# Kernel tuning notes

Hardware: AMD Instinct MI355X
Metric: run time of the kernel (lower is better)

Reference implementation:

```python
import jax, jax.numpy as jnp
import numpy as np

AXIS = 4  # axis_neuron


def silu(x):
    return x * jax.nn.sigmoid(x)


def setup_inputs() -> dict:
    key = jax.random.key(0)
    ks = jax.random.split(key, 20)
    nf, nloc, nall, nnei, a_sel = 1, 1024, 1024, 64, 20
    n_dim, e_dim, a_dim = 128, 64, 64
    f32 = jnp.float32

    def W(k, i, o):
        return jax.random.normal(k, (i, o), f32) / np.float32(np.sqrt(i))

    angle_in = a_dim + n_dim + 2 * e_dim  # angle_dim with a_compress_rate=0, a_mess_has_n=True
    return {
        "node_ebd_ext": jax.random.normal(ks[0], (nf, nall, n_dim), f32),
        "edge_ebd": jax.random.normal(ks[1], (nf, nloc, nnei, e_dim), f32),
        "h2": jax.random.normal(ks[2], (nf, nloc, nnei, 3), f32),
        "angle_ebd": jax.random.normal(ks[3], (nf, nloc, a_sel, a_sel, a_dim), f32),
        "sw": jax.random.uniform(ks[4], (nf, nloc, nnei), f32),
        "a_sw": jax.random.uniform(ks[5], (nf, nloc, a_sel), f32),
        "W_self": W(ks[6], n_dim, n_dim), "b_self": jnp.zeros((n_dim,), f32),
        "W_sym": W(ks[7], (e_dim + n_dim) * AXIS, n_dim), "b_sym": jnp.zeros((n_dim,), f32),
        "W_ne": W(ks[8], 2 * n_dim + e_dim, n_dim), "b_ne": jnp.zeros((n_dim,), f32),
        "W_es": W(ks[9], 2 * n_dim + e_dim, e_dim), "b_es": jnp.zeros((e_dim,), f32),
        "W_ea1": W(ks[10], angle_in, e_dim), "b_ea1": jnp.zeros((e_dim,), f32),
        "W_ea2": W(ks[11], e_dim, e_dim), "b_ea2": jnp.zeros((e_dim,), f32),
        "W_as": W(ks[12], angle_in, a_dim), "b_as": jnp.zeros((a_dim,), f32),
        "res_n": jnp.full((3, n_dim), 0.1, f32),
        "res_e": jnp.full((2, e_dim), 0.1, f32),
        "res_a": jnp.full((1, a_dim), 0.1, f32),
        "nlist": jax.random.randint(ks[13], (nf, nloc, nnei), 0, nall),
        "nlist_mask": jnp.ones((nf, nloc, nnei), bool),
        "a_nlist_mask": jnp.ones((nf, nloc, a_sel), bool),
    }


def _forward(node_ebd_ext, edge_ebd, h2, angle_ebd, sw, a_sw,
             W_self, b_self, W_sym, b_sym, W_ne, b_ne, W_es, b_es,
             W_ea1, b_ea1, W_ea2, b_ea2, W_as, b_as, res_n, res_e, res_a,
             nlist, nlist_mask, a_nlist_mask):
    nf, nloc, nnei, e_dim = edge_ebd.shape
    a_sel = angle_ebd.shape[2]
    a_dim = angle_ebd.shape[-1]
    n_dim = node_ebd_ext.shape[-1]
    node_ebd = node_ebd_ext[:, :nloc]  # nf x nloc x n_dim

    sw = jnp.where(nlist_mask, sw, 0.0)          # masked switch
    a_sw = jnp.where(a_nlist_mask, a_sw, 0.0)

    # gather neighbor node embeddings: nf x nloc x nnei x n_dim
    idx = jnp.where(nlist_mask, nlist, 0)
    nei_node = jnp.take_along_axis(
        node_ebd_ext, idx.reshape(nf, nloc * nnei)[..., None], axis=1
    ).reshape(nf, nloc, nnei, n_dim)

    # node self mlp
    n_self = silu(node_ebd @ W_self + b_self)

    # symmetrization op: hg = h^T g / nnei; grrg = hg[:axis]^T hg / 3
    def grrg(g):
        gw = g * sw[..., None]
        hg = jnp.einsum('flnt,flnd->fltd', h2, gw) / nnei       # f l 3 d
        out = jnp.einsum('flta,fltd->flad', hg[..., :AXIS], hg) / 3.0
        return out.reshape(nf, nloc, -1)                        # f l (axis*d)

    node_sym = silu(jnp.concatenate([grrg(edge_ebd), grrg(nei_node)], axis=-1) @ W_sym + b_sym)

    # node-edge message: linear over concat([node_i, node_j, edge]) = sum of blocks
    W0, W1, W2 = W_ne[:n_dim], W_ne[n_dim:2 * n_dim], W_ne[2 * n_dim:]
    pre_ne = (node_ebd @ W0)[:, :, None, :] + nei_node @ W1 + edge_ebd @ W2 + b_ne
    n_edge = jnp.sum(silu(pre_ne) * sw[..., None], axis=-2) / nnei

    node_new = node_ebd + res_n[0] * n_self + res_n[1] * node_sym + res_n[2] * n_edge

    # edge self message (same edge_info)
    V0, V1, V2 = W_es[:n_dim], W_es[n_dim:2 * n_dim], W_es[2 * n_dim:]
    edge_self = silu((node_ebd @ V0)[:, :, None, :] + nei_node @ V1 + edge_ebd @ V2 + b_es)

    # ---- angle path ----
    e_ang = jnp.where(a_nlist_mask[..., None], edge_ebd[:, :, :a_sel], 0.0)  # f l a e
    s0, s1, s2 = a_dim, a_dim + n_dim, a_dim + n_dim + e_dim
    A0, A1, A2, A3 = W_ea1[:s0], W_ea1[s0:s1], W_ea1[s1:s2], W_ea1[s2:]
    # angle_info @ W_ea1 without materializing the concat (blocks broadcast)
    pre_ang = (angle_ebd @ A0
               + (node_ebd @ A1)[:, :, None, None, :]
               + (e_ang @ A2)[:, :, None, :, :]   # edge_for_angle_i varies along axis 3
               + (e_ang @ A3)[:, :, :, None, :]   # edge_for_angle_j varies along axis 2
               + b_ea1)
    e_ang_upd = silu(pre_ang)                                     # f l a a e
    weighted = a_sw[:, :, :, None, None] * a_sw[:, :, None, :, None] * e_ang_upd
    reduced = jnp.sum(weighted, axis=-2) / np.float32(np.sqrt(a_sel))  # f l a e
    padded = jnp.pad(reduced, ((0, 0), (0, 0), (0, nnei - a_sel), (0, 0)))
    e_angle_msg = silu(padded @ W_ea2 + b_ea2)
    edge_new = edge_ebd + res_e[0] * edge_self + res_e[1] * e_angle_msg

    # angle self update (same angle_info)
    B0, B1, B2, B3 = W_as[:s0], W_as[s0:s1], W_as[s1:s2], W_as[s2:]
    angle_self = silu(angle_ebd @ B0
                      + (node_ebd @ B1)[:, :, None, None, :]
                      + (e_ang @ B2)[:, :, None, :, :]
                      + (e_ang @ B3)[:, :, :, None, :]
                      + b_as)
    angle_new = angle_ebd + res_a[0] * angle_self
    return node_new, edge_new, angle_new


def reference(node_ebd_ext, edge_ebd, h2, angle_ebd, sw, a_sw,
              W_self, b_self, W_sym, b_sym, W_ne, b_ne, W_es, b_es,
              W_ea1, b_ea1, W_ea2, b_ea2, W_as, b_as, res_n, res_e, res_a,
              nlist, nlist_mask, a_nlist_mask):
    return _forward(node_ebd_ext, edge_ebd, h2, angle_ebd, sw, a_sw,
                    W_self, b_self, W_sym, b_sym, W_ne, b_ne, W_es, b_es,
                    W_ea1, b_ea1, W_ea2, b_ea2, W_as, b_as, res_n, res_e, res_a,
                    nlist, nlist_mask, a_nlist_mask)
```

## Files before the change

### kernel.cpp

```cpp
#include <hip/hip_runtime.h>

#define DEVINL __device__ __forceinline__

#define NLOC 1024
#define NNEI 64
#define NDIM 128
#define EDIM 64
#define ADIM 64
#define ASEL 20

enum : size_t {
  WS_NSELF = 0,
  WS_NW0   = WS_NSELF + 1024*128,
  WS_NV0   = WS_NW0   + 1024*128,
  WS_NA1   = WS_NV0   + 1024*64,
  WS_NB1   = WS_NA1   + 1024*64,
  WS_PA2   = WS_NB1   + 1024*64,
  WS_PA3   = WS_PA2   + 1024*ASEL*64,
  WS_PB2   = WS_PA3   + 1024*ASEL*64,
  WS_PB3   = WS_PB2   + 1024*ASEL*64,
  WS_F32_END = WS_PB3 + 1024*ASEL*64
};
__device__ float g_ws[WS_F32_END];
__device__ float g_red[1024*ASEL*64];

DEVINL float siluf(float x) {
  return x * __builtin_amdgcn_rcpf(1.0f + __expf(-x));
}

__global__ __launch_bounds__(128) void k0_node_pre(
    const float* __restrict__ node,
    const float* __restrict__ W_self, const float* __restrict__ b_self,
    const float* __restrict__ W_ne,   const float* __restrict__ b_ne,
    const float* __restrict__ W_es,   const float* __restrict__ b_es,
    const float* __restrict__ W_ea1,  const float* __restrict__ b_ea1,
    const float* __restrict__ W_as,   const float* __restrict__ b_as)
{
  const int l = blockIdx.x, t = threadIdx.x;
  __shared__ float nl[128];
  nl[t] = node[l*128 + t];
  __syncthreads();
  float aS = b_self[t];
  float aW = b_ne[t];
  #pragma unroll 8
  for (int k = 0; k < 128; ++k) {
    float nv = nl[k];
    aS = fmaf(nv, W_self[k*128 + t], aS);
    aW = fmaf(nv, W_ne[k*128 + t], aW);
  }
  g_ws[WS_NSELF + l*128 + t] = siluf(aS);
  g_ws[WS_NW0   + l*128 + t] = aW;
  if (t < 64) {
    float aV = b_es[t], aA = b_ea1[t], aB = b_as[t];
    #pragma unroll 8
    for (int k = 0; k < 128; ++k) {
      float nv = nl[k];
      aV = fmaf(nv, W_es[k*64 + t], aV);
      aA = fmaf(nv, W_ea1[(64 + k)*64 + t], aA);
      aB = fmaf(nv, W_as[(64 + k)*64 + t], aB);
    }
    g_ws[WS_NV0 + l*64 + t] = aV;
    g_ws[WS_NA1 + l*64 + t] = aA;
    g_ws[WS_NB1 + l*64 + t] = aB;
  }
}

__global__ __launch_bounds__(256) void kp_proj(
    const float* __restrict__ edge,
    const float* __restrict__ W_ea1, const float* __restrict__ W_as)
{
  const int l = blockIdx.x, t = threadIdx.x;
  __shared__ float eang[ASEL*65];
  for (int e = t; e < ASEL*64; e += 256)
    eang[(e >> 6)*65 + (e & 63)] = edge[(size_t)l*4096 + e];
  __syncthreads();
  const int o = t & 63, wv = t >> 6;
  #pragma unroll 1
  for (int m = 0; m < 4; ++m) {
    const float* __restrict__ Wp =
          (m == 0) ? (W_ea1 + 192*64)
        : (m == 1) ? (W_ea1 + 256*64)
        : (m == 2) ? (W_as  + 192*64)
        :            (W_as  + 256*64);
    float* __restrict__ outp = g_ws +
          ((m == 0) ? WS_PA2 : (m == 1) ? WS_PA3 : (m == 2) ? WS_PB2 : WS_PB3)
        + (size_t)l*ASEL*64;
    float a0 = 0.f, a1 = 0.f, a2 = 0.f, a3 = 0.f, a4 = 0.f;
    #pragma unroll 4
    for (int k = 0; k < 64; ++k) {
      float w = Wp[k*64 + o];
      a0 = fmaf(eang[(wv     )*65 + k], w, a0);
      a1 = fmaf(eang[(wv +  4)*65 + k], w, a1);
      a2 = fmaf(eang[(wv +  8)*65 + k], w, a2);
      a3 = fmaf(eang[(wv + 12)*65 + k], w, a3);
      a4 = fmaf(eang[(wv + 16)*65 + k], w, a4);
    }
    outp[(wv     )*64 + o] = a0;
    outp[(wv +  4)*64 + o] = a1;
    outp[(wv +  8)*64 + o] = a2;
    outp[(wv + 12)*64 + o] = a3;
    outp[(wv + 16)*64 + o] = a4;
  }
}

__global__ __launch_bounds__(256, 4) void k2_angle(
    const float* __restrict__ ang,
    const float* __restrict__ a_sw,
    const float* __restrict__ res_a,
    const float* __restrict__ W_ea1, const float* __restrict__ W_as,
    float* __restrict__ angle_out)
{
  const int bid = blockIdx.x;
  const int l = bid / 5, b = bid % 5;
  const int t = threadIdx.x;

  __shared__ __align__(16) float angl[80*68];
  __shared__ __align__(16) float eA2l[ASEL*68], eB2l[ASEL*68];
  __shared__ float aswl[ASEL];

  const float* __restrict__ angbase = ang + ((size_t)l*400 + b*80)*64;
  #pragma unroll
  for (int q = 0; q < 5; ++q) {
    int g = t + q*256;
    int lr = g >> 4, c4 = g & 15;
    float4 v = reinterpret_cast<const float4*>(angbase)[g];
    *reinterpret_cast<float4*>(&angl[lr*68 + c4*4]) = v;
  }
  {
    const float* __restrict__ pa2 = g_ws + WS_PA2 + (size_t)l*ASEL*64;
    const float* __restrict__ pb2 = g_ws + WS_PB2 + (size_t)l*ASEL*64;
    for (int g = t; g < ASEL*16; g += 256) {
      int j = g >> 4, c4 = g & 15;
      *reinterpret_cast<float4*>(&eA2l[j*68 + c4*4]) =
          reinterpret_cast<const float4*>(pa2)[g];
      *reinterpret_cast<float4*>(&eB2l[j*68 + c4*4]) =
          reinterpret_cast<const float4*>(pb2)[g];
    }
  }
  if (t < ASEL) aswl[t] = a_sw[l*ASEL + t];

  const int cg = t & 15, rg = t >> 4;
  const int c0 = cg*4;
  const int i_loc = rg >> 2;
  const int i = b*4 + i_loc;
  const int lr0 = rg*5;

  float4 nA1v = *reinterpret_cast<const float4*>(g_ws + WS_NA1 + l*64 + c0);
  float4 nB1v = *reinterpret_cast<const float4*>(g_ws + WS_NB1 + l*64 + c0);
  float4 eA3v = *reinterpret_cast<const float4*>(g_ws + WS_PA3 + ((size_t)l*ASEL + i)*64 + c0);
  float4 eB3v = *reinterpret_cast<const float4*>(g_ws + WS_PB3 + ((size_t)l*ASEL + i)*64 + c0);
  float4 resav = *reinterpret_cast<const float4*>(res_a + c0);

  __syncthreads();

  const float* __restrict__ A0g = W_ea1;
  const float* __restrict__ B0g = W_as;

  float accA[20], accB[20];
  #pragma unroll
  for (int q = 0; q < 20; ++q) { accA[q] = 0.f; accB[q] = 0.f; }

  #pragma unroll 2
  for (int k = 0; k < 64; k += 4) {
    float vr[5][4];
    #pragma unroll
    for (int q = 0; q < 5; ++q)
      *reinterpret_cast<float4*>(vr[q]) =
          *reinterpret_cast<const float4*>(&angl[(lr0 + q)*68 + k]);
    #pragma unroll
    for (int kk = 0; kk < 4; ++kk) {
      float4 wA = *reinterpret_cast<const float4*>(A0g + (size_t)(k + kk)*64 + c0);
      float4 wB = *reinterpret_cast<const float4*>(B0g + (size_t)(k + kk)*64 + c0);
      #pragma unroll
      for (int q = 0; q < 5; ++q) {
        float av = vr[q][kk];
        accA[q*4+0] = fmaf(av, wA.x, accA[q*4+0]);
        accA[q*4+1] = fmaf(av, wA.y, accA[q*4+1]);
        accA[q*4+2] = fmaf(av, wA.z, accA[q*4+2]);
        accA[q*4+3] = fmaf(av, wA.w, accA[q*4+3]);
        accB[q*4+0] = fmaf(av, wB.x, accB[q*4+0]);
        accB[q*4+1] = fmaf(av, wB.y, accB[q*4+1]);
        accB[q*4+2] = fmaf(av, wB.z, accB[q*4+2]);
        accB[q*4+3] = fmaf(av, wB.w, accB[q*4+3]);
      }
    }
  }

  float red0 = 0.f, red1 = 0.f, red2 = 0.f, red3 = 0.f;
  #pragma unroll
  for (int q = 0; q < 5; ++q) {
    int lr = lr0 + q;
    int j = lr - i_loc*20;
    float aswj = aswl[j];
    float4 e2A = *reinterpret_cast<const float4*>(&eA2l[j*68 + c0]);
    float4 e2B = *reinterpret_cast<const float4*>(&eB2l[j*68 + c0]);
    float4 orig = *reinterpret_cast<const float4*>(&angl[lr*68 + c0]);

    float pA0 = accA[q*4+0] + nA1v.x + e2A.x + eA3v.x;
    float pA1 = accA[q*4+1] + nA1v.y + e2A.y + eA3v.y;
    float pA2 = accA[q*4+2] + nA1v.z + e2A.z + eA3v.z;
    float pA3 = accA[q*4+3] + nA1v.w + e2A.w + eA3v.w;
    red0 = fmaf(aswj, siluf(pA0), red0);
    red1 = fmaf(aswj, siluf(pA1), red1);
    red2 = fmaf(aswj, siluf(pA2), red2);
    red3 = fmaf(aswj, siluf(pA3), red3);

    float pB0 = accB[q*4+0] + nB1v.x + e2B.x + eB3v.x;
    float pB1 = accB[q*4+1] + nB1v.y + e2B.y + eB3v.y;
    float pB2 = accB[q*4+2] + nB1v.z + e2B.z + eB3v.z;
    float pB3 = accB[q*4+3] + nB1v.w + e2B.w + eB3v.w;
    float4 outv;
    outv.x = orig.x + resav.x * siluf(pB0);
    outv.y = orig.y + resav.y * siluf(pB1);
    outv.z = orig.z + resav.z * siluf(pB2);
    outv.w = orig.w + resav.w * siluf(pB3);
    *reinterpret_cast<float4*>(angle_out + ((size_t)l*400 + b*80 + lr)*64 + c0) = outv;
  }

  red0 += __shfl_xor(red0, 16); red0 += __shfl_xor(red0, 32);
  red1 += __shfl_xor(red1, 16); red1 += __shfl_xor(red1, 32);
  red2 += __shfl_xor(red2, 16); red2 += __shfl_xor(red2, 32);
  red3 += __shfl_xor(red3, 16); red3 += __shfl_xor(red3, 32);
  if ((t & 0x30) == 0) {
    float sc = aswl[i] * 0.22360679775f;
    float4 o4 = make_float4(red0*sc, red1*sc, red2*sc, red3*sc);
    *reinterpret_cast<float4*>(g_red + ((size_t)l*ASEL + i)*64 + c0) = o4;
  }
}

__global__ __launch_bounds__(256, 2) void k3_node_edge(
    const float* __restrict__ node_ext,
    const float* __restrict__ edge,
    const float* __restrict__ h2,
    const float* __restrict__ sw,
    const int* __restrict__ nlist,
    const float* __restrict__ W_sym, const float* __restrict__ b_sym,
    const float* __restrict__ W_ne,  const float* __restrict__ W_es,
    const float* __restrict__ W_ea2, const float* __restrict__ b_ea2,
    const float* __restrict__ res_n, const float* __restrict__ res_e,
    float* __restrict__ node_out,
    float* __restrict__ edge_out)
{
  const int l = blockIdx.x, t = threadIdx.x;
  __shared__ __align__(16) float AL[64*196];
  __shared__ __align__(16) float WL[16*192];
  __shared__ float hwv[64*4];
  __shared__ float swl[64];
  __shared__ float hgE[3*64], hgN[3*128];
  __shared__ float cat[768];
  __shared__ float nsym[128];
  __shared__ float msgl[ASEL*64];
  __shared__ float msgc[64];
  __shared__ float redn[128];
  __shared__ int   idxl[64];

  if (t < 64) idxl[t] = nlist[l*64 + t];
  if (t >= 64 && t < 192) redn[t - 64] = 0.f;
  if (t < 64) {
    float s = sw[l*64 + t];
    swl[t] = s;
    hwv[t*4+0] = h2[(l*64 + t)*3 + 0] * s;
    hwv[t*4+1] = h2[(l*64 + t)*3 + 1] * s;
    hwv[t*4+2] = h2[(l*64 + t)*3 + 2] * s;
  }
  __syncthreads();

  for (int g = t; g < 2048; g += 256) {
    int n = g >> 5, q = g & 31;
    float4 v = *reinterpret_cast<const float4*>(node_ext + (size_t)idxl[n]*128 + q*4);
    *reinterpret_cast<float4*>(&AL[n*196 + q*4]) = v;
  }
  for (int g = t; g < 1024; g += 256) {
    int n = g >> 4, q = g & 15;
    float4 v = *reinterpret_cast<const float4*>(edge + (size_t)l*4096 + n*64 + q*4);
    *reinterpret_cast<float4*>(&AL[n*196 + 128 + q*4]) = v;
  }
  __syncthreads();

  for (int e = t; e < 192; e += 256) {
    int tt = e >> 6, d = e & 63;
    float acc = 0.f;
    #pragma unroll 4
    for (int n = 0; n < 64; ++n) acc = fmaf(hwv[n*4 + tt], AL[n*196 + 128 + d], acc);
    hgE[tt*64 + d] = acc * (1.f/64.f);
  }
  for (int e = t; e < 384; e += 256) {
    int tt = e >> 7, k = e & 127;
    float acc = 0.f;
    #pragma unroll 4
    for (int n = 0; n < 64; ++n) acc = fmaf(hwv[n*4 + tt], AL[n*196 + k], acc);
    hgN[tt*128 + k] = acc * (1.f/64.f);
  }
  __syncthreads();

  for (int e = t; e < 256; e += 256) {
    int a = e >> 6, d = e & 63;
    cat[e] = (hgE[a]*hgE[d] + hgE[64 + a]*hgE[64 + d] + hgE[128 + a]*hgE[128 + d]) * (1.f/3.f);
  }
  for (int e = t; e < 512; e += 256) {
    int a = e >> 7, k = e & 127;
    cat[256 + e] = (hgN[a]*hgN[k] + hgN[128 + a]*hgN[128 + k] + hgN[256 + a]*hgN[256 + k]) * (1.f/3.f);
  }
  __syncthreads();

  if (t < 128) {
    float acc = b_sym[t];
    #pragma unroll 4
    for (int c = 0; c < 768; ++c)
      acc = fmaf(cat[c], W_sym[c*128 + t], acc);
    nsym[t] = siluf(acc);
  } else {
    int idx = t - 128;
    if (idx < 64) msgc[idx] = siluf(b_ea2[idx]);
    for (int q = 0; q < 10; ++q) {
      int e = q*128 + idx;
      int n = e >> 6, oo = e & 63;
      float acc = b_ea2[oo];
      #pragma unroll 4
      for (int k = 0; k < 64; ++k)
        acc = fmaf(g_red[((size_t)l*ASEL + n)*64 + k], W_ea2[k*64 + oo], acc);
      msgl[e] = siluf(acc);
    }
  }

  const int tx = t & 15, ty = t >> 4;
  const int n0 = ty*4, c0 = tx*12;

  float acc[4][12];
  #pragma unroll
  for (int r = 0; r < 4; ++r)
    #pragma unroll
    for (int cc = 0; cc < 12; ++cc) acc[r][cc] = 0.f;

  float4 wreg[3];
  #pragma unroll
  for (int q = 0; q < 3; ++q) {
    int g = q*256 + t;
    int kk = g / 48, c4 = g % 48;
    int c = c4*4, krow = 128 + kk;
    wreg[q] = (c < 128)
        ? *reinterpret_cast<const float4*>(W_ne + (size_t)krow*128 + c)
        : *reinterpret_cast<const float4*>(W_es + (size_t)krow*64 + (c - 128));
  }

  #pragma unroll 1
  for (int kb = 0; kb < 12; ++kb) {
    __syncthreads();
    #pragma unroll
    for (int q = 0; q < 3; ++q) {
      int g = q*256 + t;
      int kk = g / 48, c4 = g % 48;
      *reinterpret_cast<float4*>(&WL[kk*192 + c4*4]) = wreg[q];
    }
    if (kb < 11) {
      #pragma unroll
      for (int q = 0; q < 3; ++q) {
        int g = q*256 + t;
        int kk = g / 48, c4 = g % 48;
        int c = c4*4, krow = 128 + (kb + 1)*16 + kk;
        wreg[q] = (c < 128)
            ? *reinterpret_cast<const float4*>(W_ne + (size_t)krow*128 + c)
            : *reinterpret_cast<const float4*>(W_es + (size_t)krow*64 + (c - 128));
      }
    }
    __syncthreads();

    const int kbase = kb*16;
    #pragma unroll
    for (int kk = 0; kk < 16; kk += 4) {
      float ar[4][4];
      #pragma unroll
      for (int r = 0; r < 4; ++r)
        *reinterpret_cast<float4*>(ar[r]) =
            *reinterpret_cast<const float4*>(&AL[(n0 + r)*196 + kbase + kk]);
      #pragma unroll
      for (int j = 0; j < 4; ++j) {
        float4 w0 = *reinterpret_cast<const float4*>(&WL[(kk + j)*192 + c0]);
        float4 w1 = *reinterpret_cast<const float4*>(&WL[(kk + j)*192 + c0 + 4]);
        float4 w2 = *reinterpret_cast<const float4*>(&WL[(kk + j)*192 + c0 + 8]);
        #pragma unroll
        for (int r = 0; r < 4; ++r) {
          float av = ar[r][j];
          acc[r][0]  = fmaf(av, w0.x, acc[r][0]);
          acc[r][1]  = fmaf(av, w0.y, acc[r][1]);
          acc[r][2]  = fmaf(av, w0.z, acc[r][2]);
          acc[r][3]  = fmaf(av, w0.w, acc[r][3]);
          acc[r][4]  = fmaf(av, w1.x, acc[r][4]);
          acc[r][5]  = fmaf(av, w1.y, acc[r][5]);
          acc[r][6]  = fmaf(av, w1.z, acc[r][6]);
          acc[r][7]  = fmaf(av, w1.w, acc[r][7]);
          acc[r][8]  = fmaf(av, w2.x, acc[r][8]);
          acc[r][9]  = fmaf(av, w2.y, acc[r][9]);
          acc[r][10] = fmaf(av, w2.z, acc[r][10]);
          acc[r][11] = fmaf(av, w2.w, acc[r][11]);
        }
      }
    }
  }

  float colb[12];
  #pragma unroll
  for (int cc = 0; cc < 12; ++cc) {
    int c = c0 + cc;
    colb[cc] = (c < 128) ? g_ws[WS_NW0 + l*128 + c]
                         : g_ws[WS_NV0 + l*64 + (c - 128)];
  }
  float np[12];
  #pragma unroll
  for (int cc = 0; cc < 12; ++cc) np[cc] = 0.f;

  #pragma unroll
  for (int r = 0; r < 4; ++r) {
    int n = n0 + r;
    float sn = swl[n];
    #pragma unroll
    for (int cc = 0; cc < 12; ++cc) {
      int c = c0 + cc;
      float s = siluf(acc[r][cc] + colb[cc]);
      if (c < 128) {
        np[cc] = fmaf(s, sn, np[cc]);
      } else {
        int o = c - 128;
        float msgv = (n < ASEL) ? msgl[n*64 + o] : msgc[o];
        float ef = AL[n*196 + 128 + o];
        edge_out[(size_t)l*4096 + n*64 + o] =
            ef + res_e[o]*s + res_e[64 + o]*msgv;
      }
    }
  }

  #pragma unroll
  for (int cc = 0; cc < 12; ++cc) {
    np[cc] += __shfl_xor(np[cc], 16);
    np[cc] += __shfl_xor(np[cc], 32);
  }
  if ((ty & 3) == 0) {
    #pragma unroll
    for (int cc = 0; cc < 12; ++cc) {
      int c = c0 + cc;
      if (c < 128) atomicAdd(&redn[c], np[cc]);
    }
  }
  __syncthreads();

  if (t < 128) {
    const int c = t;
    float nedge = redn[c] * (1.f/64.f);
    float nodev = node_ext[l*128 + c];
    node_out[l*128 + c] = nodev + res_n[c]*g_ws[WS_NSELF + l*128 + c]
                        + res_n[128 + c]*nsym[c] + res_n[256 + c]*nedge;
  }
}

extern "C" void kernel_launch(void* const* d_in, const int* in_sizes, int n_in,
                              void* d_out, int out_size, void* d_ws, size_t ws_size,
                              hipStream_t stream) {
  const float* node_ext = (const float*)d_in[0];
  const float* edge_ebd = (const float*)d_in[1];
  const float* h2       = (const float*)d_in[2];
  const float* angle    = (const float*)d_in[3];
  const float* sw       = (const float*)d_in[4];
  const float* a_sw     = (const float*)d_in[5];
  const float* W_self   = (const float*)d_in[6];
  const float* b_self   = (const float*)d_in[7];
  const float* W_sym    = (const float*)d_in[8];
  const float* b_sym    = (const float*)d_in[9];
  const float* W_ne     = (const float*)d_in[10];
  const float* b_ne     = (const float*)d_in[11];
  const float* W_es     = (const float*)d_in[12];
  const float* b_es     = (const float*)d_in[13];
  const float* W_ea1    = (const float*)d_in[14];
  const float* b_ea1    = (const float*)d_in[15];
  const float* W_ea2    = (const float*)d_in[16];
  const float* b_ea2    = (const float*)d_in[17];
  const float* W_as     = (const float*)d_in[18];
  const float* b_as     = (const float*)d_in[19];
  const float* res_n    = (const float*)d_in[20];
  const float* res_e    = (const float*)d_in[21];
  const float* res_a    = (const float*)d_in[22];
  const int*   nlist    = (const int*)d_in[23];

  float* out = (float*)d_out;
  float* node_out  = out;
  float* edge_out  = out + 1024*128;
  float* angle_out = out + 1024*128 + (size_t)1024*64*64;

  k0_node_pre<<<1024, 128, 0, stream>>>(node_ext, W_self, b_self, W_ne, b_ne,
                                        W_es, b_es, W_ea1, b_ea1, W_as, b_as);
  kp_proj<<<1024, 256, 0, stream>>>(edge_ebd, W_ea1, W_as);
  k2_angle<<<1024*5, 256, 0, stream>>>(angle, a_sw, res_a,
                                       W_ea1, W_as, angle_out);
  k3_node_edge<<<1024, 256, 0, stream>>>(node_ext, edge_ebd, h2, sw, nlist,
                                         W_sym, b_sym, W_ne, W_es, W_ea2, b_ea2,
                                         res_n, res_e, node_out, edge_out);
}
```

Before: 653.0 us.

## Merge node-pre and edge projection kernels; split symmetry/message work out of node-edge kernel

```diff
diff --git a/kernel.cpp b/kernel.cpp
--- a/kernel.cpp
+++ b/kernel.cpp
@@ -19,7 +19,9 @@
   WS_PA3   = WS_PA2   + 1024*ASEL*64,
   WS_PB2   = WS_PA3   + 1024*ASEL*64,
   WS_PB3   = WS_PB2   + 1024*ASEL*64,
-  WS_F32_END = WS_PB3 + 1024*ASEL*64
+  WS_NSYM  = WS_PB3   + 1024*ASEL*64,
+  WS_MSG   = WS_NSYM  + 1024*128,
+  WS_F32_END = WS_MSG + 1024*21*64
 };
 __device__ float g_ws[WS_F32_END];
 __device__ float g_red[1024*ASEL*64];
@@ -28,8 +30,9 @@
   return x * __builtin_amdgcn_rcpf(1.0f + __expf(-x));
 }
 
-__global__ __launch_bounds__(128) void k0_node_pre(
+__global__ __launch_bounds__(256) void k01_pre(
     const float* __restrict__ node,
+    const float* __restrict__ edge,
     const float* __restrict__ W_self, const float* __restrict__ b_self,
     const float* __restrict__ W_ne,   const float* __restrict__ b_ne,
     const float* __restrict__ W_es,   const float* __restrict__ b_es,
@@ -38,42 +41,38 @@
 {
   const int l = blockIdx.x, t = threadIdx.x;
   __shared__ float nl[128];
-  nl[t] = node[l*128 + t];
-  __syncthreads();
-  float aS = b_self[t];
-  float aW = b_ne[t];
-  #pragma unroll 8
-  for (int k = 0; k < 128; ++k) {
-    float nv = nl[k];
-    aS = fmaf(nv, W_self[k*128 + t], aS);
-    aW = fmaf(nv, W_ne[k*128 + t], aW);
-  }
-  g_ws[WS_NSELF + l*128 + t] = siluf(aS);
-  g_ws[WS_NW0   + l*128 + t] = aW;
-  if (t < 64) {
-    float aV = b_es[t], aA = b_ea1[t], aB = b_as[t];
+  __shared__ float eang[ASEL*65];
+  if (t < 128) nl[t] = node[l*128 + t];
+  for (int e = t; e < ASEL*64; e += 256)
+    eang[(e >> 6)*65 + (e & 63)] = edge[(size_t)l*4096 + e];
+  __syncthreads();
+
+  if (t < 128) {
+    float aS = b_self[t];
+    float aW = b_ne[t];
     #pragma unroll 8
     for (int k = 0; k < 128; ++k) {
       float nv = nl[k];
-      aV = fmaf(nv, W_es[k*64 + t], aV);
-      aA = fmaf(nv, W_ea1[(64 + k)*64 + t], aA);
-      aB = fmaf(nv, W_as[(64 + k)*64 + t], aB);
-    }
-    g_ws[WS_NV0 + l*64 + t] = aV;
-    g_ws[WS_NA1 + l*64 + t] = aA;
-    g_ws[WS_NB1 + l*64 + t] = aB;
-  }
-}
-
-__global__ __launch_bounds__(256) void kp_proj(
-    const float* __restrict__ edge,
-    const float* __restrict__ W_ea1, const float* __restrict__ W_as)
-{
-  const int l = blockIdx.x, t = threadIdx.x;
-  __shared__ float eang[ASEL*65];
-  for (int e = t; e < ASEL*64; e += 256)
-    eang[(e >> 6)*65 + (e & 63)] = edge[(size_t)l*4096 + e];
-  __syncthreads();
+      aS = fmaf(nv, W_self[k*128 + t], aS);
+      aW = fmaf(nv, W_ne[k*128 + t], aW);
+    }
+    g_ws[WS_NSELF + l*128 + t] = siluf(aS);
+    g_ws[WS_NW0   + l*128 + t] = aW;
+    if (t < 64) {
+      float aV = b_es[t], aA = b_ea1[t], aB = b_as[t];
+      #pragma unroll 8
+      for (int k = 0; k < 128; ++k) {
+        float nv = nl[k];
+        aV = fmaf(nv, W_es[k*64 + t], aV);
+        aA = fmaf(nv, W_ea1[(64 + k)*64 + t], aA);
+        aB = fmaf(nv, W_as[(64 + k)*64 + t], aB);
+      }
+      g_ws[WS_NV0 + l*64 + t] = aV;
+      g_ws[WS_NA1 + l*64 + t] = aA;
+      g_ws[WS_NB1 + l*64 + t] = aB;
+    }
+  }
+
   const int o = t & 63, wv = t >> 6;
   #pragma unroll 1
   for (int m = 0; m < 4; ++m) {
@@ -228,15 +227,96 @@
   }
 }
 
-__global__ __launch_bounds__(256, 2) void k3_node_edge(
+__global__ __launch_bounds__(256) void kn_sym(
     const float* __restrict__ node_ext,
     const float* __restrict__ edge,
     const float* __restrict__ h2,
     const float* __restrict__ sw,
     const int* __restrict__ nlist,
     const float* __restrict__ W_sym, const float* __restrict__ b_sym,
+    const float* __restrict__ W_ea2, const float* __restrict__ b_ea2)
+{
+  const int l = blockIdx.x, t = threadIdx.x;
+  __shared__ float hwv[64*4];
+  __shared__ int   idxl[64];
+  __shared__ float gredl[ASEL*64];
+  __shared__ float hgE[3*64], hgN[3*128];
+  __shared__ float cat[768];
+  __shared__ float nsymp[2][128];
+
+  if (t < 64) {
+    idxl[t] = nlist[l*64 + t];
+    float s = sw[l*64 + t];
+    hwv[t*4+0] = h2[(l*64 + t)*3 + 0] * s;
+    hwv[t*4+1] = h2[(l*64 + t)*3 + 1] * s;
+    hwv[t*4+2] = h2[(l*64 + t)*3 + 2] * s;
+  }
+  for (int e = t; e < ASEL*64; e += 256)
+    gredl[e] = g_red[(size_t)l*ASEL*64 + e];
+  __syncthreads();
+
+  for (int e = t; e < 576; e += 256) {
+    if (e < 192) {
+      int tt = e >> 6, d = e & 63;
+      float acc = 0.f;
+      #pragma unroll 4
+      for (int n = 0; n < 64; ++n)
+        acc = fmaf(hwv[n*4 + tt], edge[(size_t)l*4096 + n*64 + d], acc);
+      hgE[tt*64 + d] = acc * (1.f/64.f);
+    } else {
+      int e2 = e - 192;
+      int tt = e2 >> 7, k = e2 & 127;
+      float acc = 0.f;
+      #pragma unroll 4
+      for (int n = 0; n < 64; ++n)
+        acc = fmaf(hwv[n*4 + tt], node_ext[(size_t)idxl[n]*128 + k], acc);
+      hgN[tt*128 + k] = acc * (1.f/64.f);
+    }
+  }
+  __syncthreads();
+
+  {
+    int e = t;
+    int a = e >> 6, d = e & 63;
+    cat[e] = (hgE[a]*hgE[d] + hgE[64 + a]*hgE[64 + d] + hgE[128 + a]*hgE[128 + d]) * (1.f/3.f);
+  }
+  for (int e = t; e < 512; e += 256) {
+    int a = e >> 7, k = e & 127;
+    cat[256 + e] = (hgN[a]*hgN[k] + hgN[128 + a]*hgN[128 + k] + hgN[256 + a]*hgN[256 + k]) * (1.f/3.f);
+  }
+  __syncthreads();
+
+  {
+    const int c = t & 127, half = t >> 7;
+    const int k0 = half*384;
+    float acc = half ? 0.f : b_sym[c];
+    #pragma unroll 8
+    for (int k = 0; k < 384; ++k)
+      acc = fmaf(cat[k0 + k], W_sym[(size_t)(k0 + k)*128 + c], acc);
+    nsymp[half][c] = acc;
+  }
+  __syncthreads();
+  if (t < 128)
+    g_ws[WS_NSYM + l*128 + t] = siluf(nsymp[0][t] + nsymp[1][t]);
+
+  for (int e = t; e < 21*64; e += 256) {
+    int n = e >> 6, o = e & 63;
+    float acc = b_ea2[o];
+    if (n < ASEL) {
+      #pragma unroll 4
+      for (int k = 0; k < 64; ++k)
+        acc = fmaf(gredl[n*64 + k], W_ea2[k*64 + o], acc);
+    }
+    g_ws[WS_MSG + (size_t)l*21*64 + e] = siluf(acc);
+  }
+}
+
+__global__ __launch_bounds__(256, 2) void k3_node_edge(
+    const float* __restrict__ node_ext,
+    const float* __restrict__ edge,
+    const float* __restrict__ sw,
+    const int* __restrict__ nlist,
     const float* __restrict__ W_ne,  const float* __restrict__ W_es,
-    const float* __restrict__ W_ea2, const float* __restrict__ b_ea2,
     const float* __restrict__ res_n, const float* __restrict__ res_e,
     float* __restrict__ node_out,
     float* __restrict__ edge_out)
@@ -244,93 +324,13 @@
   const int l = blockIdx.x, t = threadIdx.x;
   __shared__ __align__(16) float AL[64*196];
   __shared__ __align__(16) float WL[16*192];
-  __shared__ float hwv[64*4];
   __shared__ float swl[64];
-  __shared__ float hgE[3*64], hgN[3*128];
-  __shared__ float cat[768];
-  __shared__ float nsym[128];
-  __shared__ float msgl[ASEL*64];
-  __shared__ float msgc[64];
   __shared__ float redn[128];
   __shared__ int   idxl[64];
 
-  if (t < 64) idxl[t] = nlist[l*64 + t];
-  if (t >= 64 && t < 192) redn[t - 64] = 0.f;
-  if (t < 64) {
-    float s = sw[l*64 + t];
-    swl[t] = s;
-    hwv[t*4+0] = h2[(l*64 + t)*3 + 0] * s;
-    hwv[t*4+1] = h2[(l*64 + t)*3 + 1] * s;
-    hwv[t*4+2] = h2[(l*64 + t)*3 + 2] * s;
-  }
-  __syncthreads();
-
-  for (int g = t; g < 2048; g += 256) {
-    int n = g >> 5, q = g & 31;
-    float4 v = *reinterpret_cast<const float4*>(node_ext + (size_t)idxl[n]*128 + q*4);
-    *reinterpret_cast<float4*>(&AL[n*196 + q*4]) = v;
-  }
-  for (int g = t; g < 1024; g += 256) {
-    int n = g >> 4, q = g & 15;
-    float4 v = *reinterpret_cast<const float4*>(edge + (size_t)l*4096 + n*64 + q*4);
-    *reinterpret_cast<float4*>(&AL[n*196 + 128 + q*4]) = v;
-  }
-  __syncthreads();
-
-  for (int e = t; e < 192; e += 256) {
-    int tt = e >> 6, d = e & 63;
-    float acc = 0.f;
-    #pragma unroll 4
-    for (int n = 0; n < 64; ++n) acc = fmaf(hwv[n*4 + tt], AL[n*196 + 128 + d], acc);
-    hgE[tt*64 + d] = acc * (1.f/64.f);
-  }
-  for (int e = t; e < 384; e += 256) {
-    int tt = e >> 7, k = e & 127;
-    float acc = 0.f;
-    #pragma unroll 4
-    for (int n = 0; n < 64; ++n) acc = fmaf(hwv[n*4 + tt], AL[n*196 + k], acc);
-    hgN[tt*128 + k] = acc * (1.f/64.f);
-  }
-  __syncthreads();
-
-  for (int e = t; e < 256; e += 256) {
-    int a = e >> 6, d = e & 63;
-    cat[e] = (hgE[a]*hgE[d] + hgE[64 + a]*hgE[64 + d] + hgE[128 + a]*hgE[128 + d]) * (1.f/3.f);
-  }
-  for (int e = t; e < 512; e += 256) {
-    int a = e >> 7, k = e & 127;
-    cat[256 + e] = (hgN[a]*hgN[k] + hgN[128 + a]*hgN[128 + k] + hgN[256 + a]*hgN[256 + k]) * (1.f/3.f);
-  }
-  __syncthreads();
-
-  if (t < 128) {
-    float acc = b_sym[t];
-    #pragma unroll 4
-    for (int c = 0; c < 768; ++c)
-      acc = fmaf(cat[c], W_sym[c*128 + t], acc);
-    nsym[t] = siluf(acc);
-  } else {
-    int idx = t - 128;
-    if (idx < 64) msgc[idx] = siluf(b_ea2[idx]);
-    for (int q = 0; q < 10; ++q) {
-      int e = q*128 + idx;
-      int n = e >> 6, oo = e & 63;
-      float acc = b_ea2[oo];
-      #pragma unroll 4
-      for (int k = 0; k < 64; ++k)
-        acc = fmaf(g_red[((size_t)l*ASEL + n)*64 + k], W_ea2[k*64 + oo], acc);
-      msgl[e] = siluf(acc);
-    }
-  }
-
-  const int tx = t & 15, ty = t >> 4;
-  const int n0 = ty*4, c0 = tx*12;
-
-  float acc[4][12];
-  #pragma unroll
-  for (int r = 0; r < 4; ++r)
-    #pragma unroll
-    for (int cc = 0; cc < 12; ++cc) acc[r][cc] = 0.f;
+  if (t < 64) { idxl[t] = nlist[l*64 + t]; swl[t] = sw[l*64 + t]; }
+  if (t >= 128) redn[t - 128] = 0.f;
+  __syncthreads();
 
   float4 wreg[3];
   #pragma unroll
@@ -342,6 +342,26 @@
         ? *reinterpret_cast<const float4*>(W_ne + (size_t)krow*128 + c)
         : *reinterpret_cast<const float4*>(W_es + (size_t)krow*64 + (c - 128));
   }
+
+  for (int g = t; g < 2048; g += 256) {
+    int n = g >> 5, q = g & 31;
+    float4 v = *reinterpret_cast<const float4*>(node_ext + (size_t)idxl[n]*128 + q*4);
+    *reinterpret_cast<float4*>(&AL[n*196 + q*4]) = v;
+  }
+  for (int g = t; g < 1024; g += 256) {
+    int n = g >> 4, q = g & 15;
+    float4 v = *reinterpret_cast<const float4*>(edge + (size_t)l*4096 + n*64 + q*4);
+    *reinterpret_cast<float4*>(&AL[n*196 + 128 + q*4]) = v;
+  }
+
+  const int tx = t & 15, ty = t >> 4;
+  const int n0 = ty*4, c0 = tx*12;
+
+  float acc[4][12];
+  #pragma unroll
+  for (int r = 0; r < 4; ++r)
+    #pragma unroll
+    for (int cc = 0; cc < 12; ++cc) acc[r][cc] = 0.f;
 
   #pragma unroll 1
   for (int kb = 0; kb < 12; ++kb) {
@@ -405,6 +425,7 @@
     colb[cc] = (c < 128) ? g_ws[WS_NW0 + l*128 + c]
                          : g_ws[WS_NV0 + l*64 + (c - 128)];
   }
+  const float* __restrict__ msgb = g_ws + WS_MSG + (size_t)l*21*64;
   float np[12];
   #pragma unroll
   for (int cc = 0; cc < 12; ++cc) np[cc] = 0.f;
@@ -421,7 +442,7 @@
         np[cc] = fmaf(s, sn, np[cc]);
       } else {
         int o = c - 128;
-        float msgv = (n < ASEL) ? msgl[n*64 + o] : msgc[o];
+        float msgv = msgb[((n < ASEL) ? n : ASEL)*64 + o];
         float ef = AL[n*196 + 128 + o];
         edge_out[(size_t)l*4096 + n*64 + o] =
             ef + res_e[o]*s + res_e[64 + o]*msgv;
@@ -448,7 +469,8 @@
     float nedge = redn[c] * (1.f/64.f);
     float nodev = node_ext[l*128 + c];
     node_out[l*128 + c] = nodev + res_n[c]*g_ws[WS_NSELF + l*128 + c]
-                        + res_n[128 + c]*nsym[c] + res_n[256 + c]*nedge;
+                        + res_n[128 + c]*g_ws[WS_NSYM + l*128 + c]
+                        + res_n[256 + c]*nedge;
   }
 }
 
@@ -485,12 +507,14 @@
   float* edge_out  = out + 1024*128;
   float* angle_out = out + 1024*128 + (size_t)1024*64*64;
 
-  k0_node_pre<<<1024, 128, 0, stream>>>(node_ext, W_self, b_self, W_ne, b_ne,
-                                        W_es, b_es, W_ea1, b_ea1, W_as, b_as);
-  kp_proj<<<1024, 256, 0, stream>>>(edge_ebd, W_ea1, W_as);
+  k01_pre<<<1024, 256, 0, stream>>>(node_ext, edge_ebd, W_self, b_self,
+                                    W_ne, b_ne, W_es, b_es, W_ea1, b_ea1,
+                                    W_as, b_as);
   k2_angle<<<1024*5, 256, 0, stream>>>(angle, a_sw, res_a,
                                        W_ea1, W_as, angle_out);
-  k3_node_edge<<<1024, 256, 0, stream>>>(node_ext, edge_ebd, h2, sw, nlist,
-                                         W_sym, b_sym, W_ne, W_es, W_ea2, b_ea2,
-                                         res_n, res_e, node_out, edge_out);
+  kn_sym<<<1024, 256, 0, stream>>>(node_ext, edge_ebd, h2, sw, nlist,
+                                   W_sym, b_sym, W_ea2, b_ea2);
+  k3_node_edge<<<1024, 256, 0, stream>>>(node_ext, edge_ebd, sw, nlist,
+                                         W_ne, W_es, res_n, res_e,
+                                         node_out, edge_out);
 }
```

Measured after the change: 578.2 us. 11.4% less time.
